# Optimization experiments

Measured on AMD Instinct MI355X. Metric: run time of the kernel, lower is better.

The kernel has to match this reference:

```python
import jax, jax.numpy as jnp
import numpy as np

B, N, C, H, I, ID = 4, 1024, 1024, 16, 77, 768
HD = C // H
HID = 4 * C


def _ln(t, w, b):
    m = jnp.mean(t, axis=-1, keepdims=True)
    v = jnp.mean((t - m) ** 2, axis=-1, keepdims=True)
    return (t - m) * jax.lax.rsqrt(v + 1e-5) * w + b


def _gelu(t):
    return jax.nn.gelu(t, approximate=False)


def setup_inputs() -> dict:
    key = jax.random.key(0)
    ks = iter(jax.random.split(key, 16))

    def nrm(shape, s=0.02):
        return jax.random.normal(next(ks), shape, jnp.float32) * s

    return {
        'x': jax.random.normal(next(ks), (B, N, C), jnp.float32),
        'instruct_states': jax.random.normal(next(ks), (B, I, ID), jnp.float32),
        'norm1_w': jnp.ones((C,), jnp.float32), 'norm1_b': jnp.zeros((C,), jnp.float32),
        'qkv_w': nrm((3 * C, C)),
        'q_bias': jnp.zeros((C,), jnp.float32), 'v_bias': jnp.zeros((C,), jnp.float32),
        'proj_w': nrm((C, C)), 'proj_b': jnp.zeros((C,), jnp.float32),
        'gamma_1': jnp.full((C,), 1e-5, jnp.float32), 'gamma_2': jnp.full((C,), 1e-5, jnp.float32),
        'norm2_w': jnp.ones((C,), jnp.float32), 'norm2_b': jnp.zeros((C,), jnp.float32),
        'fc1_w': nrm((HID, C)), 'fc1_b': jnp.zeros((HID,), jnp.float32),
        'fc2_w': nrm((C, HID)), 'fc2_b': jnp.zeros((C,), jnp.float32),
        'pfc1_w': nrm((HID, C)), 'pfc1_b': jnp.zeros((HID,), jnp.float32),
        'pfc2_w': nrm((C, HID)), 'pfc2_b': jnp.zeros((C,), jnp.float32),
        'parallel_gate': jnp.full((1,), 0.1, jnp.float32),
        'ir_ln_w': jnp.ones((ID,), jnp.float32), 'ir_ln_b': jnp.zeros((ID,), jnp.float32),
        'ir_l1_w': nrm((C, ID)), 'ir_l1_b': jnp.zeros((C,), jnp.float32),
        'ir_l2_w': nrm((C, C)), 'ir_l2_b': jnp.zeros((C,), jnp.float32),
    }


def reference(x, instruct_states, norm1_w, norm1_b, qkv_w, q_bias, v_bias,
              proj_w, proj_b, gamma_1, gamma_2, norm2_w, norm2_b,
              fc1_w, fc1_b, fc2_w, fc2_b, pfc1_w, pfc1_b, pfc2_w, pfc2_b,
              parallel_gate, ir_ln_w, ir_ln_b, ir_l1_w, ir_l1_b, ir_l2_w, ir_l2_b):
    # instruct_dim_reduce: LN -> Linear -> GELU -> Linear
    kv = _ln(instruct_states, ir_ln_w, ir_ln_b)
    kv = _gelu(kv @ ir_l1_w.T + ir_l1_b) @ ir_l2_w.T + ir_l2_b  # [B, I, C]

    xn = _ln(x, norm1_w, norm1_b)                               # [B, N, C]
    cat = jnp.concatenate([kv, xn], axis=1)                     # [B, I+N, C]
    S = I + N

    qkv_bias = jnp.concatenate([q_bias, jnp.zeros_like(v_bias), v_bias])
    qkv = (cat @ qkv_w.T + qkv_bias).reshape(B, S, 3, H, HD)
    q = qkv[:, :, 0].transpose(0, 2, 1, 3)                      # [B, H, S, HD]
    k = qkv[:, :, 1].transpose(0, 2, 1, 3)
    v = qkv[:, :, 2].transpose(0, 2, 1, 3)

    # only visual queries, keys/values over instructions + visual tokens
    q = q[:, :, I:, :] * (HD ** -0.5)                           # [B, H, N, HD]
    attn = jnp.einsum('bhqd,bhkd->bhqk', q, k)                  # [B, H, N, S]
    attn = jax.nn.softmax(attn, axis=-1)
    o = jnp.einsum('bhqk,bhkd->bqhd', attn, v).reshape(B, N, C)
    o = o @ proj_w.T + proj_b

    x = x + gamma_1 * o                                         # LayerScale residual

    y = _ln(x, norm2_w, norm2_b)
    mlp = _gelu(y @ fc1_w.T + fc1_b) @ fc2_w.T + fc2_b
    pmlp = _gelu(y @ pfc1_w.T + pfc1_b) @ pfc2_w.T + pfc2_b
    x = x + gamma_2 * mlp + parallel_gate * pmlp
    return x
```

## Files before the change

kernel.cpp:

```cpp
#include <hip/hip_runtime.h>
#include <cstdint>

#define Bv   4
#define Nv   1024
#define Cv   1024
#define Hv   16
#define Iv   77
#define IDv  768
#define HDv  64
#define HIDv 4096
#define Sv   (Iv + Nv)
#define BIv  (Bv * Iv)
#define BSv  (Bv * Sv)
#define BNv  (Bv * Nv)
#define SPADv 1152

typedef __bf16 bf16x8_t __attribute__((ext_vector_type(8)));
typedef float  f32x4_t  __attribute__((ext_vector_type(4)));
typedef unsigned short us8_t __attribute__((ext_vector_type(8)));
typedef long  l2_t  __attribute__((ext_vector_type(2)));
typedef int   i32x4_t __attribute__((ext_vector_type(4)));
typedef int   i32x8_t __attribute__((ext_vector_type(8)));

__device__ inline f32x4_t zero4() { f32x4_t z; z[0]=0.f; z[1]=0.f; z[2]=0.f; z[3]=0.f; return z; }

__device__ inline unsigned short f2bf(float f) {
    unsigned int u = __builtin_bit_cast(unsigned int, f);
    u = (u + 0x7fffu + ((u >> 16) & 1u)) >> 16;
    return (unsigned short)u;
}
__device__ inline float bf2f(unsigned short u) {
    return __builtin_bit_cast(float, ((unsigned int)u) << 16);
}
__device__ inline unsigned int f4_fp8(float a, float b, float c, float d) {
    int v = __builtin_amdgcn_cvt_pk_fp8_f32(a, b, 0, false);
    v = __builtin_amdgcn_cvt_pk_fp8_f32(c, d, v, true);
    return (unsigned int)v;
}

__device__ inline float gelu_f(float x) {
    float u = 0.7978845608f * x * (1.0f + 0.044715f * x * x);
    float e = __expf(2.0f * u);
    float t = 1.0f - 2.0f / (e + 1.0f);
    return 0.5f * x * (1.0f + t);
}

__device__ inline void gload_lds16(const void* g, void* l) {
    __builtin_amdgcn_global_load_lds(
        (__attribute__((address_space(1))) void*)(unsigned long long)g,
        (__attribute__((address_space(3))) void*)(unsigned long long)l,
        16, 0, 0);
}

__device__ inline i32x8_t frag32(const unsigned char* p0, const unsigned char* p1) {
    i32x4_t lo = *(const i32x4_t*)p0;
    i32x4_t hi = *(const i32x4_t*)p1;
    i32x8_t r;
    r[0] = lo[0]; r[1] = lo[1]; r[2] = lo[2]; r[3] = lo[3];
    r[4] = hi[0]; r[5] = hi[1]; r[6] = hi[2]; r[7] = hi[3];
    return r;
}

#define PIPE_WAIT(N) do { \
    asm volatile("s_waitcnt vmcnt(" #N ")" ::: "memory"); \
    __builtin_amdgcn_s_barrier(); \
    __builtin_amdgcn_sched_barrier(0); \
} while (0)
#define PIPE_RELEASE() do { \
    __builtin_amdgcn_sched_barrier(0); \
    __builtin_amdgcn_s_barrier(); \
} while (0)

__global__ __launch_bounds__(256) void cvt8_kernel(
        const float* s0, const float* s1, const float* s2, const float* s3,
        const float* s4, const float* s5, const float* s6, const float* s7,
        void* d0, void* d1, void* d2, void* d3,
        void* d4, void* d5, void* d6, void* d7,
        const float* g1, const float* g2, const float* gate) {
    long i = (long)blockIdx.x * 256 + threadIdx.x;
    const float* src; void* dst; long off;
    const float* sptr = nullptr; int K4 = 1; float wmul = 1.0f; bool f8 = false;
    if (i < 2097152) {
        if (i < 786432)       { src = s0; dst = d0; off = i; }
        else if (i < 1048576) { src = s1; dst = d1; off = i - 786432;  sptr = g1; K4 = 256; }
        else                  { src = s2; dst = d2; off = i - 1048576; f8 = true; wmul = 32.f; }
    } else if (i < 4194304) {
        if (i < 3145728)      { src = s3; dst = d3; off = i - 2097152; f8 = true; wmul = 32.f; sptr = g2; K4 = 1024; }
        else                  { src = s4; dst = d4; off = i - 3145728; f8 = true; wmul = 32.f; }
    } else {
        if (i < 5242880)      { src = s5; dst = d5; off = i - 4194304; f8 = true; wmul = 32.f; sptr = gate; K4 = 0x7fffffff; }
        else if (i < 5439488) { src = s6; dst = d6; off = i - 5242880; }
        else                  { src = s7; dst = d7; off = i - 5439488; }
    }
    float sc = (sptr ? sptr[(int)(off / K4)] : 1.0f) * wmul;
    float4 v = ((const float4*)src)[off];
    if (f8) {
        ((unsigned int*)dst)[off] = f4_fp8(v.x * sc, v.y * sc, v.z * sc, v.w * sc);
    } else {
        ushort4 o = {f2bf(v.x * sc), f2bf(v.y * sc), f2bf(v.z * sc), f2bf(v.w * sc)};
        ((ushort4*)dst)[off] = o;
    }
}

__global__ __launch_bounds__(256) void bias_prep_kernel(
        const float* __restrict__ qb, const float* __restrict__ vb,
        const float* __restrict__ fc2b, const float* __restrict__ pfc2b,
        const float* __restrict__ projb_in,
        const float* __restrict__ fc1b, const float* __restrict__ pfc1b,
        const float* __restrict__ g1, const float* __restrict__ g2,
        const float* __restrict__ gate,
        float* __restrict__ qkvb, float* __restrict__ bfuse,
        float* __restrict__ projb, float* __restrict__ bcat) {
    int i = blockIdx.x * 256 + threadIdx.x;
    if (i < 3 * Cv) {
        float v = 0.f;
        if (i < Cv) v = qb[i];
        else if (i >= 2 * Cv) v = vb[i - 2 * Cv];
        qkvb[i] = v;
    } else if (i < 4 * Cv) {
        int n = i - 3 * Cv;
        bfuse[n] = g2[n] * fc2b[n] + gate[0] * pfc2b[n];
    } else if (i < 5 * Cv) {
        int n = i - 4 * Cv;
        projb[n] = g1[n] * projb_in[n];
    } else if (i < 13 * Cv) {
        int j = i - 5 * Cv;
        bcat[j] = (j < HIDv) ? fc1b[j] : pfc1b[j - HIDv];
    }
}

__global__ __launch_bounds__(256) void scatter_kv_kernel(const unsigned short* __restrict__ kv,
                                                         unsigned short* __restrict__ cat) {
    int r = blockIdx.x;
    int b = r / Iv, i = r % Iv;
    const uint2* src = (const uint2*)(kv + (size_t)r * Cv);
    uint2* dst = (uint2*)(cat + (size_t)(b * Sv + i) * Cv);
    dst[threadIdx.x] = src[threadIdx.x];
}

template <int F8>
__global__ __launch_bounds__(256) void ln_kernel(const float* __restrict__ in,
                                                 const float* __restrict__ w,
                                                 const float* __restrict__ bvec,
                                                 void* __restrict__ out,
                                                 int cols, float invcols,
                                                 int div_, int stride_, int off_) {
    const int r = blockIdx.x;
    const int tid = threadIdx.x;
    const float* row = in + (size_t)r * cols;
    float s = 0.f, s2 = 0.f;
    for (int c = tid * 4; c < cols; c += 1024) {
        float4 v = *(const float4*)(row + c);
        s  += v.x + v.y + v.z + v.w;
        s2 += v.x * v.x + v.y * v.y + v.z * v.z + v.w * v.w;
    }
#pragma unroll
    for (int o2 = 32; o2 > 0; o2 >>= 1) { s += __shfl_down(s, o2); s2 += __shfl_down(s2, o2); }
    __shared__ float sh[10];
    const int lane = tid & 63, wave = tid >> 6;
    if (lane == 0) { sh[wave] = s; sh[4 + wave] = s2; }
    __syncthreads();
    if (tid == 0) {
        float S1 = sh[0] + sh[1] + sh[2] + sh[3];
        float S2 = sh[4] + sh[5] + sh[6] + sh[7];
        float mean = S1 * invcols;
        float var  = S2 * invcols - mean * mean;
        sh[8] = mean;
        sh[9] = rsqrtf(var + 1e-5f);
    }
    __syncthreads();
    const float mean = sh[8], rstd = sh[9];
    const size_t orow = (size_t)((r / div_) * stride_ + (r % div_) + off_) * cols;
    for (int c = tid * 4; c < cols; c += 1024) {
        float4 v  = *(const float4*)(row + c);
        float4 wv = *(const float4*)(w + c);
        float4 bv = *(const float4*)(bvec + c);
        float o0 = (v.x - mean) * rstd * wv.x + bv.x;
        float o1 = (v.y - mean) * rstd * wv.y + bv.y;
        float o2 = (v.z - mean) * rstd * wv.z + bv.z;
        float o3 = (v.w - mean) * rstd * wv.w + bv.w;
        if constexpr (F8) {
            *(unsigned int*)((unsigned char*)out + orow + c) =
                f4_fp8(o0 * 16.f, o1 * 16.f, o2 * 16.f, o3 * 16.f);
        } else {
            ushort4 o = {f2bf(o0), f2bf(o1), f2bf(o2), f2bf(o3)};
            *(ushort4*)((unsigned short*)out + orow + c) = o;
        }
    }
}

template <int MODE>
__global__ __launch_bounds__(256) void gemm_bf16_kernel(
        const unsigned short* __restrict__ A,
        const unsigned short* __restrict__ W,
        const float* __restrict__ bias,
        unsigned short* __restrict__ outp,
        int M, int N, int K) {
    __shared__ unsigned short As[2][128 * 32];
    __shared__ unsigned short Bs[2][128 * 32];
    const int tid  = threadIdx.x;
    const int lane = tid & 63;
    const int wave = tid >> 6;
    const int m16  = lane & 15;
    const int g4   = lane >> 4;
    const int n0 = blockIdx.x * 128;
    const int m0 = blockIdx.y * 128;
    const int wm = (wave >> 1) * 64;
    const int wn = (wave & 1) * 64;

    const int r0  = tid >> 2;
    const int cc0 = (tid & 3) * 8;
    int am0 = m0 + r0;       if (am0 > M - 1) am0 = M - 1;
    int am1 = m0 + r0 + 64;  if (am1 > M - 1) am1 = M - 1;
    const unsigned short* agp0 = A + (size_t)am0 * K + cc0;
    const unsigned short* agp1 = A + (size_t)am1 * K + cc0;
    const unsigned short* bgp0 = W + (size_t)(n0 + r0) * K + cc0;
    const unsigned short* bgp1 = W + (size_t)(n0 + r0 + 64) * K + cc0;

    f32x4_t acc[4][4];
#pragma unroll
    for (int a = 0; a < 4; ++a)
#pragma unroll
        for (int bb = 0; bb < 4; ++bb) acc[a][bb] = zero4();

    auto stage = [&](int buf) {
        gload_lds16(agp0, &As[buf][wave * 512]);
        gload_lds16(agp1, &As[buf][2048 + wave * 512]);
        gload_lds16(bgp0, &Bs[buf][wave * 512]);
        gload_lds16(bgp1, &Bs[buf][2048 + wave * 512]);
        agp0 += 32; agp1 += 32; bgp0 += 32; bgp1 += 32;
    };

    auto body = [&](int cur) {
        bf16x8_t xf[4], wf[4];
#pragma unroll
        for (int bb = 0; bb < 4; ++bb)
            xf[bb] = *(const bf16x8_t*)&As[cur][(wm + bb * 16 + m16) * 32 + g4 * 8];
#pragma unroll
        for (int a = 0; a < 4; ++a)
            wf[a] = *(const bf16x8_t*)&Bs[cur][(wn + a * 16 + m16) * 32 + g4 * 8];
#pragma unroll
        for (int a = 0; a < 4; ++a)
#pragma unroll
            for (int bb = 0; bb < 4; ++bb)
                acc[a][bb] = __builtin_amdgcn_mfma_f32_16x16x32_bf16(wf[a], xf[bb], acc[a][bb], 0, 0, 0);
    };

    const int NIT = K >> 5;
    stage(0);
    stage(1);
    for (int it = 0; it < NIT - 1; ++it) {
        const int cur = it & 1;
        PIPE_WAIT(4);
        body(cur);
        PIPE_RELEASE();
        if (it + 2 < NIT) stage(cur);
    }
    PIPE_WAIT(0);
    body((NIT - 1) & 1);

#pragma unroll
    for (int a = 0; a < 4; ++a) {
        const int cb = n0 + wn + a * 16 + g4 * 4;
        const float4 bv4 = *(const float4*)(bias + cb);
#pragma unroll
        for (int bb = 0; bb < 4; ++bb) {
            const int r = m0 + wm + bb * 16 + m16;
            if (r < M) {
                const size_t idx = (size_t)r * N + cb;
                const float v0 = acc[a][bb][0] + bv4.x;
                const float v1 = acc[a][bb][1] + bv4.y;
                const float v2 = acc[a][bb][2] + bv4.z;
                const float v3 = acc[a][bb][3] + bv4.w;
                if constexpr (MODE == 0) {
                    ushort4 o = {f2bf(v0), f2bf(v1), f2bf(v2), f2bf(v3)};
                    *(ushort4*)(outp + idx) = o;
                } else {
                    ushort4 o = {f2bf(gelu_f(v0)), f2bf(gelu_f(v1)),
                                 f2bf(gelu_f(v2)), f2bf(gelu_f(v3))};
                    *(ushort4*)(outp + idx) = o;
                }
            }
        }
    }
}

__global__ __launch_bounds__(256) void gemm_splitk_kernel(
        const unsigned short* __restrict__ A1,
        const unsigned short* __restrict__ W1,
        unsigned short* __restrict__ parts,
        int M, int N, int KA, int Kc) {
    __shared__ unsigned short As[2][128 * 32];
    __shared__ unsigned short Bs[2][128 * 32];
    const int tid  = threadIdx.x;
    const int lane = tid & 63;
    const int wave = tid >> 6;
    const int m16  = lane & 15;
    const int g4   = lane >> 4;
    const int bid = blockIdx.x;
    const int xcd = bid & 7, l = bid >> 3;
    const int by = (xcd << 2) | (l & 3);
    const int rr = l >> 2;
    const int bx = rr & 7;
    const int z  = rr >> 3;
    const int n0 = bx * 128;
    const int m0 = by * 128;
    const int wm = (wave >> 1) * 64;
    const int wn = (wave & 1) * 64;
    const int k0 = z * Kc;

    const int r0  = tid >> 2;
    const int cc0 = (tid & 3) * 8;
    const unsigned short* agp0 = A1 + (size_t)(m0 + r0) * KA + k0 + cc0;
    const unsigned short* agp1 = A1 + (size_t)(m0 + r0 + 64) * KA + k0 + cc0;
    const unsigned short* bgp0 = W1 + (size_t)(n0 + r0) * KA + k0 + cc0;
    const unsigned short* bgp1 = W1 + (size_t)(n0 + r0 + 64) * KA + k0 + cc0;

    f32x4_t acc[4][4];
#pragma unroll
    for (int a = 0; a < 4; ++a)
#pragma unroll
        for (int bb = 0; bb < 4; ++bb) acc[a][bb] = zero4();

    auto stage = [&](int buf) {
        gload_lds16(agp0, &As[buf][wave * 512]);
        gload_lds16(agp1, &As[buf][2048 + wave * 512]);
        gload_lds16(bgp0, &Bs[buf][wave * 512]);
        gload_lds16(bgp1, &Bs[buf][2048 + wave * 512]);
        agp0 += 32; agp1 += 32; bgp0 += 32; bgp1 += 32;
    };

    auto body = [&](int cur) {
        bf16x8_t xf[4], wf[4];
#pragma unroll
        for (int bb = 0; bb < 4; ++bb)
            xf[bb] = *(const bf16x8_t*)&As[cur][(wm + bb * 16 + m16) * 32 + g4 * 8];
#pragma unroll
        for (int a = 0; a < 4; ++a)
            wf[a] = *(const bf16x8_t*)&Bs[cur][(wn + a * 16 + m16) * 32 + g4 * 8];
#pragma unroll
        for (int a = 0; a < 4; ++a)
#pragma unroll
            for (int bb = 0; bb < 4; ++bb)
                acc[a][bb] = __builtin_amdgcn_mfma_f32_16x16x32_bf16(wf[a], xf[bb], acc[a][bb], 0, 0, 0);
    };

    const int NIT = Kc >> 5;
    stage(0);
    stage(1);
    for (int it = 0; it < NIT - 1; ++it) {
        const int cur = it & 1;
        PIPE_WAIT(4);
        body(cur);
        PIPE_RELEASE();
        if (it + 2 < NIT) stage(cur);
    }
    PIPE_WAIT(0);
    body((NIT - 1) & 1);

    unsigned short* pz = parts + (size_t)z * M * N;
#pragma unroll
    for (int a = 0; a < 4; ++a) {
        const int cb = n0 + wn + a * 16 + g4 * 4;
#pragma unroll
        for (int bb = 0; bb < 4; ++bb) {
            const int r = m0 + wm + bb * 16 + m16;
            const size_t idx = (size_t)r * N + cb;
            ushort4 o = {f2bf(acc[a][bb][0]), f2bf(acc[a][bb][1]),
                         f2bf(acc[a][bb][2]), f2bf(acc[a][bb][3])};
            *(ushort4*)(pz + idx) = o;
        }
    }
}

__global__ __launch_bounds__(256) void gemm_fp8_gelu_kernel(
        const unsigned char* __restrict__ A,
        const unsigned char* __restrict__ W,
        const float* __restrict__ bias,
        unsigned char* __restrict__ outp,
        int M, int N, int K) {
    __shared__ unsigned char As[2][128 * 128];
    __shared__ unsigned char Bs[2][128 * 128];
    const int tid  = threadIdx.x;
    const int lane = tid & 63;
    const int wave = tid >> 6;
    const int m16  = lane & 15;
    const int g4   = lane >> 4;
    const int bid = blockIdx.x;
    const int xcd = bid & 7, l = bid >> 3;
    const int by = (xcd << 2) | (l & 3);
    const int bx = l >> 2;
    const int n0 = bx * 128;
    const int m0 = by * 128;
    const int wm = (wave >> 1) * 64;
    const int wn = (wave & 1) * 64;

    const int rowin = tid >> 3;
    const int sslot = (tid & 7) ^ (rowin & 7);
    const unsigned char* agp = A + (size_t)(m0 + rowin) * K + sslot * 16;
    const unsigned char* bgp = W + (size_t)(n0 + rowin) * K + sslot * 16;

    const int sw = m16 & 7;
    const int ra0 = ((2 * g4) ^ sw) * 16;
    const int ra1 = ((2 * g4 + 1) ^ sw) * 16;

    f32x4_t acc[4][4];
#pragma unroll
    for (int a = 0; a < 4; ++a)
#pragma unroll
        for (int bb = 0; bb < 4; ++bb) acc[a][bb] = zero4();

    auto stage = [&](int buf) {
#pragma unroll
        for (int j = 0; j < 4; ++j) {
            gload_lds16(agp + (size_t)j * 32 * K, &As[buf][j * 4096 + wave * 1024]);
            gload_lds16(bgp + (size_t)j * 32 * K, &Bs[buf][j * 4096 + wave * 1024]);
        }
        agp += 128; bgp += 128;
    };

    stage(0);
    const int NIT = K >> 7;
    for (int it = 0; it < NIT; ++it) {
        const int cur = it & 1;
        __syncthreads();
        if (it + 1 < NIT) stage(cur ^ 1);
        i32x8_t xv[4], wv[4];
#pragma unroll
        for (int bb = 0; bb < 4; ++bb) {
            const unsigned char* rb = &As[cur][(wm + bb * 16 + m16) * 128];
            xv[bb] = frag32(rb + ra0, rb + ra1);
        }
#pragma unroll
        for (int a = 0; a < 4; ++a) {
            const unsigned char* rb = &Bs[cur][(wn + a * 16 + m16) * 128];
            wv[a] = frag32(rb + ra0, rb + ra1);
        }
#pragma unroll
        for (int a = 0; a < 4; ++a)
#pragma unroll
            for (int bb = 0; bb < 4; ++bb)
                acc[a][bb] = __builtin_amdgcn_mfma_scale_f32_16x16x128_f8f6f4(
                    wv[a], xv[bb], acc[a][bb], 0, 0, 0, 0x7f7f7f7f, 0, 0x7f7f7f7f);
    }

    const float ds = 1.0f / 512.0f;
#pragma unroll
    for (int a = 0; a < 4; ++a) {
        const int cb = n0 + wn + a * 16 + g4 * 4;
        const float4 bv4 = *(const float4*)(bias + cb);
#pragma unroll
        for (int bb = 0; bb < 4; ++bb) {
            const int r = m0 + wm + bb * 16 + m16;
            const size_t idx = (size_t)r * N + cb;
            unsigned int pk = f4_fp8(gelu_f(acc[a][bb][0] * ds + bv4.x) * 16.f,
                                     gelu_f(acc[a][bb][1] * ds + bv4.y) * 16.f,
                                     gelu_f(acc[a][bb][2] * ds + bv4.z) * 16.f,
                                     gelu_f(acc[a][bb][3] * ds + bv4.w) * 16.f);
            *(unsigned int*)(outp + idx) = pk;
        }
    }
}

__global__ __launch_bounds__(256) void gemm_fp8_splitk_kernel(
        const unsigned char* __restrict__ A1,
        const unsigned char* __restrict__ W1,
        const unsigned char* __restrict__ A2,
        const unsigned char* __restrict__ W2,
        unsigned short* __restrict__ parts,
        int M, int N, int lda, int ldw, int Kc, int zsplit) {
    __shared__ unsigned char As[2][128 * 128];
    __shared__ unsigned char Bs[2][128 * 128];
    const int tid  = threadIdx.x;
    const int lane = tid & 63;
    const int wave = tid >> 6;
    const int m16  = lane & 15;
    const int g4   = lane >> 4;
    const int bid = blockIdx.x;
    const int xcd = bid & 7, l = bid >> 3;
    const int by = (xcd << 2) | (l & 3);
    const int rr = l >> 2;
    const int bx = rr & 7;
    const int z  = rr >> 3;
    const int n0 = bx * 128;
    const int m0 = by * 128;
    const int wm = (wave >> 1) * 64;
    const int wn = (wave & 1) * 64;

    const unsigned char* A = (z < zsplit) ? A1 : A2;
    const unsigned char* W = (z < zsplit) ? W1 : W2;
    const int k0 = (z % zsplit) * Kc;

    const int rowin = tid >> 3;
    const int sslot = (tid & 7) ^ (rowin & 7);
    const unsigned char* agp = A + (size_t)(m0 + rowin) * lda + k0 + sslot * 16;
    const unsigned char* bgp = W + (size_t)(n0 + rowin) * ldw + k0 + sslot * 16;

    const int sw = m16 & 7;
    const int ra0 = ((2 * g4) ^ sw) * 16;
    const int ra1 = ((2 * g4 + 1) ^ sw) * 16;

    f32x4_t acc[4][4];
#pragma unroll
    for (int a = 0; a < 4; ++a)
#pragma unroll
        for (int bb = 0; bb < 4; ++bb) acc[a][bb] = zero4();

    auto stage = [&](int buf) {
#pragma unroll
        for (int j = 0; j < 4; ++j) {
            gload_lds16(agp + (size_t)j * 32 * lda, &As[buf][j * 4096 + wave * 1024]);
            gload_lds16(bgp + (size_t)j * 32 * ldw, &Bs[buf][j * 4096 + wave * 1024]);
        }
        agp += 128; bgp += 128;
    };

    stage(0);
    const int NIT = Kc >> 7;
    for (int it = 0; it < NIT; ++it) {
        const int cur = it & 1;
        __syncthreads();
        if (it + 1 < NIT) stage(cur ^ 1);
        i32x8_t xv[4], wv[4];
#pragma unroll
        for (int bb = 0; bb < 4; ++bb) {
            const unsigned char* rb = &As[cur][(wm + bb * 16 + m16) * 128];
            xv[bb] = frag32(rb + ra0, rb + ra1);
        }
#pragma unroll
        for (int a = 0; a < 4; ++a) {
            const unsigned char* rb = &Bs[cur][(wn + a * 16 + m16) * 128];
            wv[a] = frag32(rb + ra0, rb + ra1);
        }
#pragma unroll
        for (int a = 0; a < 4; ++a)
#pragma unroll
            for (int bb = 0; bb < 4; ++bb)
                acc[a][bb] = __builtin_amdgcn_mfma_scale_f32_16x16x128_f8f6f4(
                    wv[a], xv[bb], acc[a][bb], 0, 0, 0, 0x7f7f7f7f, 0, 0x7f7f7f7f);
    }

    unsigned short* pz = parts + (size_t)z * M * N;
    const float ds = 1.0f / 512.0f;
#pragma unroll
    for (int a = 0; a < 4; ++a) {
        const int cb = n0 + wn + a * 16 + g4 * 4;
#pragma unroll
        for (int bb = 0; bb < 4; ++bb) {
            const int r = m0 + wm + bb * 16 + m16;
            const size_t idx = (size_t)r * N + cb;
            ushort4 o = {f2bf(acc[a][bb][0] * ds), f2bf(acc[a][bb][1] * ds),
                         f2bf(acc[a][bb][2] * ds), f2bf(acc[a][bb][3] * ds)};
            *(ushort4*)(pz + idx) = o;
        }
    }
}

template <int NP>
__global__ __launch_bounds__(256) void reduce_kernel(
        const unsigned short* __restrict__ parts,
        const float* __restrict__ resid,
        const float* __restrict__ bias,
        float* __restrict__ out, int MN, int N4mask) {
    int i = blockIdx.x * 256 + threadIdx.x;
    if (i * 4 >= MN) return;
    float4 res = ((const float4*)resid)[i];
    float4 bv  = *(const float4*)(bias + (i & N4mask) * 4);
    float4 o = {res.x + bv.x, res.y + bv.y, res.z + bv.z, res.w + bv.w};
#pragma unroll
    for (int z = 0; z < NP; ++z) {
        ushort4 u = ((const ushort4*)(parts + (size_t)z * MN))[i];
        o.x += bf2f(u.x); o.y += bf2f(u.y); o.z += bf2f(u.z); o.w += bf2f(u.w);
    }
    ((float4*)out)[i] = o;
}

__global__ __launch_bounds__(256) void vtrans_kernel(const unsigned short* __restrict__ qkv,
                                                     unsigned short* __restrict__ vt) {
    __shared__ unsigned short Vs[64 * 64];
    const int stile = blockIdx.x;
    const int bh = blockIdx.y;
    const int b = bh >> 4, h = bh & 15;
    const int tid = threadIdx.x;
#pragma unroll
    for (int j = 0; j < 2; ++j) {
        int c = j * 256 + tid;
        int r = c >> 3, d8 = (c & 7) * 8;
        int s = stile * 64 + r;
        uint4 v = {0u, 0u, 0u, 0u};
        if (s < Sv) v = *(const uint4*)(qkv + ((size_t)(b * Sv + s) * 3 + 2) * Cv + h * 64 + d8);
        *(uint4*)&Vs[r * 64 + d8] = v;
    }
    __syncthreads();
    const int d  = tid >> 2;
    const int p0 = (tid & 3) * 16;
    unsigned short tmp[16];
#pragma unroll
    for (int e = 0; e < 16; ++e) {
        int p = p0 + e;
        int s_local = (p & 32) + 16 * ((p >> 2) & 1) + 4 * ((p & 31) >> 3) + (p & 3);
        tmp[e] = Vs[s_local * 64 + d];
    }
    unsigned short* dst = vt + ((size_t)bh * 64 + d) * SPADv + stile * 64 + p0;
    *(uint4*)dst       = *(const uint4*)&tmp[0];
    *(uint4*)(dst + 8) = *(const uint4*)&tmp[8];
}

__global__ __launch_bounds__(256) void attn_kernel(const unsigned short* __restrict__ qkv,
                                                   const unsigned short* __restrict__ vt,
                                                   unsigned short* __restrict__ o) {
    __shared__ unsigned short Qs[64 * 64];
    __shared__ unsigned short Ks[2][64 * 64];
    __shared__ unsigned short Vts[2][64 * 64];

    const int tid  = threadIdx.x;
    const int lane = tid & 63;
    const int wave = tid >> 6;
    const int m16  = lane & 15;
    const int g4   = lane >> 4;
    const int qt = blockIdx.x;
    const int bh = blockIdx.y;
    const int b = bh >> 4, h = bh & 15;

    const int lr = lane >> 3;
    const int csw = ((lane & 7) ^ lr) * 8;
    const int sw7 = m16 & 7;

#pragma unroll
    for (int j = 0; j < 2; ++j) {
        int r = wave * 16 + j * 8 + lr;
        int s = Iv + qt * 64 + r;
        gload_lds16(qkv + ((size_t)(b * Sv + s) * 3) * Cv + h * 64 + csw,
                    &Qs[(wave * 16 + j * 8) * 64]);
    }

    auto stage_kv = [&](int st, int buf) {
#pragma unroll
        for (int j = 0; j < 2; ++j) {
            int r = wave * 16 + j * 8 + lr;
            int s = st * 64 + r; if (s > Sv - 1) s = Sv - 1;
            gload_lds16(qkv + ((size_t)(b * Sv + s) * 3 + 1) * Cv + h * 64 + csw,
                        &Ks[buf][(wave * 16 + j * 8) * 64]);
            gload_lds16(vt + ((size_t)bh * 64 + r) * SPADv + st * 64 + csw,
                        &Vts[buf][(wave * 16 + j * 8) * 64]);
        }
    };

    f32x4_t oacc[4];
#pragma unroll
    for (int dt = 0; dt < 4; ++dt) oacc[dt] = zero4();
    float m_run = -1e30f, l_run = 0.f;

    stage_kv(0, 0);
    __syncthreads();

    const bf16x8_t qf0 = *(const bf16x8_t*)&Qs[(wave * 16 + m16) * 64 + ((g4 ^ sw7) * 8)];
    const bf16x8_t qf1 = *(const bf16x8_t*)&Qs[(wave * 16 + m16) * 64 + (((4 + g4) ^ sw7) * 8)];

    const int NT = (Sv + 63) / 64;
    for (int st = 0; st < NT; ++st) {
        const int cur = st & 1;
        if (st + 1 < NT) stage_kv(st + 1, cur ^ 1);

        f32x4_t sc[4];
#pragma unroll
        for (int kt = 0; kt < 4; ++kt) {
            bf16x8_t k0 = *(const bf16x8_t*)&Ks[cur][(kt * 16 + m16) * 64 + ((g4 ^ sw7) * 8)];
            bf16x8_t k1 = *(const bf16x8_t*)&Ks[cur][(kt * 16 + m16) * 64 + (((4 + g4) ^ sw7) * 8)];
            f32x4_t z = zero4();
            z = __builtin_amdgcn_mfma_f32_16x16x32_bf16(k0, qf0, z, 0, 0, 0);
            z = __builtin_amdgcn_mfma_f32_16x16x32_bf16(k1, qf1, z, 0, 0, 0);
            sc[kt] = z;
        }

        float mx = -1e30f;
#pragma unroll
        for (int kt = 0; kt < 4; ++kt)
#pragma unroll
            for (int r = 0; r < 4; ++r) {
                int key = st * 64 + kt * 16 + g4 * 4 + r;
                float v = sc[kt][r] * 0.125f;
                v = (key < Sv) ? v : -1e30f;
                sc[kt][r] = v;
                mx = fmaxf(mx, v);
            }
        mx = fmaxf(mx, __shfl_xor(mx, 16));
        mx = fmaxf(mx, __shfl_xor(mx, 32));
        const float mnew  = fmaxf(m_run, mx);
        const float alpha = __expf(m_run - mnew);
        m_run = mnew;
        float sum = 0.f;
#pragma unroll
        for (int kt = 0; kt < 4; ++kt)
#pragma unroll
            for (int r = 0; r < 4; ++r) {
                float p = __expf(sc[kt][r] - mnew);
                sc[kt][r] = p;
                sum += p;
            }
        sum += __shfl_xor(sum, 16);
        sum += __shfl_xor(sum, 32);
        l_run = l_run * alpha + sum;
#pragma unroll
        for (int dt = 0; dt < 4; ++dt) oacc[dt] *= alpha;

        us8_t pu0, pu1;
#pragma unroll
        for (int j = 0; j < 8; ++j) {
            pu0[j] = f2bf(sc[(j >> 2)][j & 3]);
            pu1[j] = f2bf(sc[2 + (j >> 2)][j & 3]);
        }
        const bf16x8_t pf0 = __builtin_bit_cast(bf16x8_t, pu0);
        const bf16x8_t pf1 = __builtin_bit_cast(bf16x8_t, pu1);

#pragma unroll
        for (int dt = 0; dt < 4; ++dt) {
            bf16x8_t v0 = *(const bf16x8_t*)&Vts[cur][(dt * 16 + m16) * 64 + ((g4 ^ sw7) * 8)];
            bf16x8_t v1 = *(const bf16x8_t*)&Vts[cur][(dt * 16 + m16) * 64 + (((4 + g4) ^ sw7) * 8)];
            oacc[dt] = __builtin_amdgcn_mfma_f32_16x16x32_bf16(v0, pf0, oacc[dt], 0, 0, 0);
            oacc[dt] = __builtin_amdgcn_mfma_f32_16x16x32_bf16(v1, pf1, oacc[dt], 0, 0, 0);
        }
        __syncthreads();
    }

    const float inv = 1.0f / l_run;
    const int q = qt * 64 + wave * 16 + m16;
    const size_t row = (size_t)(b * Nv + q) * Cv + h * 64;
#pragma unroll
    for (int dt = 0; dt < 4; ++dt) {
        ushort4 o4 = {f2bf(oacc[dt][0] * inv), f2bf(oacc[dt][1] * inv),
                      f2bf(oacc[dt][2] * inv), f2bf(oacc[dt][3] * inv)};
        *(ushort4*)&o[row + dt * 16 + g4 * 4] = o4;
    }
}

extern "C" void kernel_launch(void* const* d_in, const int* in_sizes, int n_in,
                              void* d_out, int out_size, void* d_ws, size_t ws_size,
                              hipStream_t stream) {
    (void)in_sizes; (void)n_in; (void)out_size; (void)ws_size;
    const float* x       = (const float*)d_in[0];
    const float* instr   = (const float*)d_in[1];
    const float* norm1_w = (const float*)d_in[2];
    const float* norm1_b = (const float*)d_in[3];
    const float* qkv_w   = (const float*)d_in[4];
    const float* q_bias  = (const float*)d_in[5];
    const float* v_bias  = (const float*)d_in[6];
    const float* proj_w  = (const float*)d_in[7];
    const float* proj_b  = (const float*)d_in[8];
    const float* gamma_1 = (const float*)d_in[9];
    const float* gamma_2 = (const float*)d_in[10];
    const float* norm2_w = (const float*)d_in[11];
    const float* norm2_b = (const float*)d_in[12];
    const float* fc1_w   = (const float*)d_in[13];
    const float* fc1_b   = (const float*)d_in[14];
    const float* fc2_w   = (const float*)d_in[15];
    const float* fc2_b   = (const float*)d_in[16];
    const float* pfc1_w  = (const float*)d_in[17];
    const float* pfc1_b  = (const float*)d_in[18];
    const float* pfc2_w  = (const float*)d_in[19];
    const float* pfc2_b  = (const float*)d_in[20];
    const float* gate    = (const float*)d_in[21];
    const float* ir_ln_w = (const float*)d_in[22];
    const float* ir_ln_b = (const float*)d_in[23];
    const float* ir_l1_w = (const float*)d_in[24];
    const float* ir_l1_b = (const float*)d_in[25];
    const float* ir_l2_w = (const float*)d_in[26];
    const float* ir_l2_b = (const float*)d_in[27];
    float* out = (float*)d_out;

    char* ws = (char*)d_ws;
    size_t off = 0;
    auto alloc = [&](size_t bytes) -> char* {
        char* p = ws + off;
        off += (bytes + 255) & ~(size_t)255;
        return p;
    };
    unsigned short* w_qkv  = (unsigned short*)alloc((size_t)3 * Cv * Cv * 2);
    unsigned short* w_proj = (unsigned short*)alloc((size_t)Cv * Cv * 2);
    unsigned char*  w_mlp1 = (unsigned char*)alloc((size_t)2 * HIDv * Cv);
    unsigned char*  w_fc2  = (unsigned char*)alloc((size_t)Cv * HIDv);
    unsigned char*  w_pfc2 = (unsigned char*)alloc((size_t)Cv * HIDv);
    unsigned short* w_ir1  = (unsigned short*)alloc((size_t)Cv * IDv * 2);
    unsigned short* w_ir2  = (unsigned short*)alloc((size_t)Cv * Cv * 2);
    float*          qkvb   = (float*)alloc((size_t)3 * Cv * 4);
    float*          bfuse  = (float*)alloc((size_t)Cv * 4);
    float*          projb  = (float*)alloc((size_t)Cv * 4);
    float*          bcat   = (float*)alloc((size_t)2 * HIDv * 4);
    unsigned short* irln   = (unsigned short*)alloc((size_t)BIv * IDv * 2);
    unsigned short* h1     = (unsigned short*)alloc((size_t)BIv * Cv * 2);
    unsigned short* kvtmp  = (unsigned short*)alloc((size_t)BIv * Cv * 2);
    unsigned short* cat    = (unsigned short*)alloc((size_t)BSv * Cv * 2);
    unsigned short* qkvbuf = (unsigned short*)alloc((size_t)BSv * 3 * Cv * 2);
    unsigned short* obuf   = (unsigned short*)alloc((size_t)BNv * Cv * 2);
    float*          x1     = (float*)alloc((size_t)BNv * Cv * 4);
    unsigned char*  ybuf8  = (unsigned char*)alloc((size_t)BNv * Cv);
    unsigned char*  gbufA  = (unsigned char*)alloc((size_t)BNv * 2 * HIDv);
    unsigned short* fpart  = (unsigned short*)alloc((size_t)4 * BNv * Cv * 2);
    unsigned short* vt     = (unsigned short*)gbufA;
    unsigned short* ppart  = cat;

    cvt8_kernel<<<22272, 256, 0, stream>>>(qkv_w, proj_w, fc1_w, fc2_w, pfc1_w, pfc2_w,
                                           ir_l1_w, ir_l2_w,
                                           w_qkv, w_proj, w_mlp1, w_fc2,
                                           w_mlp1 + (size_t)HIDv * Cv, w_pfc2,
                                           w_ir1, w_ir2,
                                           gamma_1, gamma_2, gate);

    bias_prep_kernel<<<52, 256, 0, stream>>>(q_bias, v_bias, fc2_b, pfc2_b, proj_b,
                                             fc1_b, pfc1_b,
                                             gamma_1, gamma_2, gate,
                                             qkvb, bfuse, projb, bcat);

    ln_kernel<0><<<BIv, 256, 0, stream>>>(instr, ir_ln_w, ir_ln_b, irln,
                                          IDv, 1.0f / IDv, 1 << 28, 0, 0);
    ln_kernel<0><<<BNv, 256, 0, stream>>>(x, norm1_w, norm1_b, cat,
                                          Cv, 1.0f / Cv, Nv, Sv, Iv);
    gemm_bf16_kernel<1><<<dim3(Cv / 128, (BIv + 127) / 128), 256, 0, stream>>>(
        irln, w_ir1, ir_l1_b, h1, BIv, Cv, IDv);
    gemm_bf16_kernel<0><<<dim3(Cv / 128, (BIv + 127) / 128), 256, 0, stream>>>(
        h1, w_ir2, ir_l2_b, kvtmp, BIv, Cv, Cv);
    scatter_kv_kernel<<<BIv, 256, 0, stream>>>(kvtmp, cat);

    gemm_bf16_kernel<0><<<dim3(3 * Cv / 128, (BSv + 127) / 128), 256, 0, stream>>>(
        cat, w_qkv, qkvb, qkvbuf, BSv, 3 * Cv, Cv);

    vtrans_kernel<<<dim3(18, Bv * Hv), 256, 0, stream>>>(qkvbuf, vt);
    attn_kernel<<<dim3(Nv / 64, Bv * Hv), 256, 0, stream>>>(qkvbuf, vt, obuf);

    gemm_splitk_kernel<<<1024, 256, 0, stream>>>(
        obuf, w_proj, ppart, BNv, Cv, Cv, Cv / 4);
    reduce_kernel<4><<<(BNv * Cv / 4 + 255) / 256, 256, 0, stream>>>(
        ppart, x, projb, x1, BNv * Cv, Cv / 4 - 1);

    ln_kernel<1><<<BNv, 256, 0, stream>>>(x1, norm2_w, norm2_b, ybuf8,
                                          Cv, 1.0f / Cv, 1 << 28, 0, 0);

    gemm_fp8_gelu_kernel<<<2048, 256, 0, stream>>>(
        ybuf8, w_mlp1, bcat, gbufA, BNv, 2 * HIDv, Cv);

    gemm_fp8_splitk_kernel<<<1024, 256, 0, stream>>>(
        gbufA, w_fc2, gbufA + HIDv, w_pfc2, fpart,
        BNv, Cv, 2 * HIDv, HIDv, HIDv / 2, 2);
    reduce_kernel<4><<<(BNv * Cv / 4 + 255) / 256, 256, 0, stream>>>(
        fpart, x1, bfuse, out, BNv * Cv, Cv / 4 - 1);
}
```

Before: 483.2 us.

## Switch QKV and output-projection GEMMs from bf16 to fp8 MFMA

Converts the QKV and proj weights to scaled fp8. The LN1 output, the scattered instruction kv and the attention output are now written as fp8 with a x16 scale. A new fp8 GEMM with bf16 output handles the QKV projection, and the proj GEMM reuses the existing fp8 split-k kernel. gamma_1 is moved from the weight conversion into a new reduce_scale kernel. This halves operand bytes and uses the higher-throughput fp8 MFMA, at the cost of lower precision on the attention path.

```diff
diff --git a/kernel.cpp b/kernel.cpp
--- a/kernel.cpp
+++ b/kernel.cpp
@@ -77,12 +77,13 @@
         void* d0, void* d1, void* d2, void* d3,
         void* d4, void* d5, void* d6, void* d7,
         const float* g1, const float* g2, const float* gate) {
+    (void)g1;
     long i = (long)blockIdx.x * 256 + threadIdx.x;
     const float* src; void* dst; long off;
     const float* sptr = nullptr; int K4 = 1; float wmul = 1.0f; bool f8 = false;
     if (i < 2097152) {
-        if (i < 786432)       { src = s0; dst = d0; off = i; }
-        else if (i < 1048576) { src = s1; dst = d1; off = i - 786432;  sptr = g1; K4 = 256; }
+        if (i < 786432)       { src = s0; dst = d0; off = i; f8 = true; wmul = 32.f; }
+        else if (i < 1048576) { src = s1; dst = d1; off = i - 786432;  f8 = true; wmul = 32.f; }
         else                  { src = s2; dst = d2; off = i - 1048576; f8 = true; wmul = 32.f; }
     } else if (i < 4194304) {
         if (i < 3145728)      { src = s3; dst = d3; off = i - 2097152; f8 = true; wmul = 32.f; sptr = g2; K4 = 1024; }
@@ -130,12 +131,14 @@
 }
 
 __global__ __launch_bounds__(256) void scatter_kv_kernel(const unsigned short* __restrict__ kv,
-                                                         unsigned short* __restrict__ cat) {
+                                                         unsigned char* __restrict__ cat) {
     int r = blockIdx.x;
     int b = r / Iv, i = r % Iv;
-    const uint2* src = (const uint2*)(kv + (size_t)r * Cv);
-    uint2* dst = (uint2*)(cat + (size_t)(b * Sv + i) * Cv);
-    dst[threadIdx.x] = src[threadIdx.x];
+    const ushort4* src = (const ushort4*)(kv + (size_t)r * Cv);
+    unsigned int* dst = (unsigned int*)(cat + (size_t)(b * Sv + i) * Cv);
+    ushort4 u = src[threadIdx.x];
+    dst[threadIdx.x] = f4_fp8(bf2f(u.x) * 16.f, bf2f(u.y) * 16.f,
+                              bf2f(u.z) * 16.f, bf2f(u.w) * 16.f);
 }
 
 template <int F8>
@@ -285,36 +288,37 @@
     }
 }
 
-__global__ __launch_bounds__(256) void gemm_splitk_kernel(
-        const unsigned short* __restrict__ A1,
-        const unsigned short* __restrict__ W1,
-        unsigned short* __restrict__ parts,
-        int M, int N, int KA, int Kc) {
-    __shared__ unsigned short As[2][128 * 32];
-    __shared__ unsigned short Bs[2][128 * 32];
+__global__ __launch_bounds__(256) void gemm_fp8_bf16out_kernel(
+        const unsigned char* __restrict__ A,
+        const unsigned char* __restrict__ W,
+        const float* __restrict__ bias,
+        unsigned short* __restrict__ outp,
+        int M, int N, int K) {
+    __shared__ unsigned char As[2][128 * 128];
+    __shared__ unsigned char Bs[2][128 * 128];
     const int tid  = threadIdx.x;
     const int lane = tid & 63;
     const int wave = tid >> 6;
     const int m16  = lane & 15;
     const int g4   = lane >> 4;
-    const int bid = blockIdx.x;
-    const int xcd = bid & 7, l = bid >> 3;
-    const int by = (xcd << 2) | (l & 3);
-    const int rr = l >> 2;
-    const int bx = rr & 7;
-    const int z  = rr >> 3;
-    const int n0 = bx * 128;
-    const int m0 = by * 128;
+    const int n0 = blockIdx.x * 128;
+    const int m0 = blockIdx.y * 128;
     const int wm = (wave >> 1) * 64;
     const int wn = (wave & 1) * 64;
-    const int k0 = z * Kc;
-
-    const int r0  = tid >> 2;
-    const int cc0 = (tid & 3) * 8;
-    const unsigned short* agp0 = A1 + (size_t)(m0 + r0) * KA + k0 + cc0;
-    const unsigned short* agp1 = A1 + (size_t)(m0 + r0 + 64) * KA + k0 + cc0;
-    const unsigned short* bgp0 = W1 + (size_t)(n0 + r0) * KA + k0 + cc0;
-    const unsigned short* bgp1 = W1 + (size_t)(n0 + r0 + 64) * KA + k0 + cc0;
+
+    const int rowin = tid >> 3;
+    const int sslot = (tid & 7) ^ (rowin & 7);
+    const unsigned char* agp[4];
+#pragma unroll
+    for (int j = 0; j < 4; ++j) {
+        int gr = m0 + j * 32 + rowin; if (gr > M - 1) gr = M - 1;
+        agp[j] = A + (size_t)gr * K + sslot * 16;
+    }
+    const unsigned char* bgp = W + (size_t)(n0 + rowin) * K + sslot * 16;
+
+    const int sw = m16 & 7;
+    const int ra0 = ((2 * g4) ^ sw) * 16;
+    const int ra1 = ((2 * g4 + 1) ^ sw) * 16;
 
     f32x4_t acc[4][4];
 #pragma unroll
@@ -323,52 +327,56 @@
         for (int bb = 0; bb < 4; ++bb) acc[a][bb] = zero4();
 
     auto stage = [&](int buf) {
-        gload_lds16(agp0, &As[buf][wave * 512]);
-        gload_lds16(agp1, &As[buf][2048 + wave * 512]);
-        gload_lds16(bgp0, &Bs[buf][wave * 512]);
-        gload_lds16(bgp1, &Bs[buf][2048 + wave * 512]);
-        agp0 += 32; agp1 += 32; bgp0 += 32; bgp1 += 32;
+#pragma unroll
+        for (int j = 0; j < 4; ++j) {
+            gload_lds16(agp[j], &As[buf][j * 4096 + wave * 1024]);
+            gload_lds16(bgp + (size_t)j * 32 * K, &Bs[buf][j * 4096 + wave * 1024]);
+            agp[j] += 128;
+        }
+        bgp += 128;
     };
 
-    auto body = [&](int cur) {
-        bf16x8_t xf[4], wf[4];
-#pragma unroll
-        for (int bb = 0; bb < 4; ++bb)
-            xf[bb] = *(const bf16x8_t*)&As[cur][(wm + bb * 16 + m16) * 32 + g4 * 8];
+    stage(0);
+    const int NIT = K >> 7;
+    for (int it = 0; it < NIT; ++it) {
+        const int cur = it & 1;
+        __syncthreads();
+        if (it + 1 < NIT) stage(cur ^ 1);
+        i32x8_t xv[4], wv[4];
+#pragma unroll
+        for (int bb = 0; bb < 4; ++bb) {
+            const unsigned char* rb = &As[cur][(wm + bb * 16 + m16) * 128];
+            xv[bb] = frag32(rb + ra0, rb + ra1);
+        }
+#pragma unroll
+        for (int a = 0; a < 4; ++a) {
+            const unsigned char* rb = &Bs[cur][(wn + a * 16 + m16) * 128];
+            wv[a] = frag32(rb + ra0, rb + ra1);
+        }
 #pragma unroll
         for (int a = 0; a < 4; ++a)
-            wf[a] = *(const bf16x8_t*)&Bs[cur][(wn + a * 16 + m16) * 32 + g4 * 8];
-#pragma unroll
-        for (int a = 0; a < 4; ++a)
 #pragma unroll
             for (int bb = 0; bb < 4; ++bb)
-                acc[a][bb] = __builtin_amdgcn_mfma_f32_16x16x32_bf16(wf[a], xf[bb], acc[a][bb], 0, 0, 0);
-    };
-
-    const int NIT = Kc >> 5;
-    stage(0);
-    stage(1);
-    for (int it = 0; it < NIT - 1; ++it) {
-        const int cur = it & 1;
-        PIPE_WAIT(4);
-        body(cur);
-        PIPE_RELEASE();
-        if (it + 2 < NIT) stage(cur);
-    }
-    PIPE_WAIT(0);
-    body((NIT - 1) & 1);
-
-    unsigned short* pz = parts + (size_t)z * M * N;
+                acc[a][bb] = __builtin_amdgcn_mfma_scale_f32_16x16x128_f8f6f4(
+                    wv[a], xv[bb], acc[a][bb], 0, 0, 0, 0x7f7f7f7f, 0, 0x7f7f7f7f);
+    }
+
+    const float ds = 1.0f / 512.0f;
 #pragma unroll
     for (int a = 0; a < 4; ++a) {
         const int cb = n0 + wn + a * 16 + g4 * 4;
+        const float4 bv4 = *(const float4*)(bias + cb);
 #pragma unroll
         for (int bb = 0; bb < 4; ++bb) {
             const int r = m0 + wm + bb * 16 + m16;
-            const size_t idx = (size_t)r * N + cb;
-            ushort4 o = {f2bf(acc[a][bb][0]), f2bf(acc[a][bb][1]),
-                         f2bf(acc[a][bb][2]), f2bf(acc[a][bb][3])};
-            *(ushort4*)(pz + idx) = o;
+            if (r < M) {
+                const size_t idx = (size_t)r * N + cb;
+                ushort4 o = {f2bf(acc[a][bb][0] * ds + bv4.x),
+                             f2bf(acc[a][bb][1] * ds + bv4.y),
+                             f2bf(acc[a][bb][2] * ds + bv4.z),
+                             f2bf(acc[a][bb][3] * ds + bv4.w)};
+                *(ushort4*)(outp + idx) = o;
+            }
         }
     }
 }
@@ -575,6 +583,30 @@
     ((float4*)out)[i] = o;
 }
 
+template <int NP>
+__global__ __launch_bounds__(256) void reduce_scale_kernel(
+        const unsigned short* __restrict__ parts,
+        const float* __restrict__ resid,
+        const float* __restrict__ bias,
+        const float* __restrict__ scale,
+        float* __restrict__ out, int MN, int N4mask) {
+    int i = blockIdx.x * 256 + threadIdx.x;
+    if (i * 4 >= MN) return;
+    float4 res = ((const float4*)resid)[i];
+    const int c4 = (i & N4mask) * 4;
+    float4 bv = *(const float4*)(bias + c4);
+    float4 sc = *(const float4*)(scale + c4);
+    float sx = 0.f, sy = 0.f, sz = 0.f, sw = 0.f;
+#pragma unroll
+    for (int z = 0; z < NP; ++z) {
+        ushort4 u = ((const ushort4*)(parts + (size_t)z * MN))[i];
+        sx += bf2f(u.x); sy += bf2f(u.y); sz += bf2f(u.z); sw += bf2f(u.w);
+    }
+    float4 o = {res.x + bv.x + sc.x * sx, res.y + bv.y + sc.y * sy,
+                res.z + bv.z + sc.z * sz, res.w + bv.w + sc.w * sw};
+    ((float4*)out)[i] = o;
+}
+
 __global__ __launch_bounds__(256) void vtrans_kernel(const unsigned short* __restrict__ qkv,
                                                      unsigned short* __restrict__ vt) {
     __shared__ unsigned short Vs[64 * 64];
@@ -608,7 +640,7 @@
 
 __global__ __launch_bounds__(256) void attn_kernel(const unsigned short* __restrict__ qkv,
                                                    const unsigned short* __restrict__ vt,
-                                                   unsigned short* __restrict__ o) {
+                                                   unsigned char* __restrict__ o) {
     __shared__ unsigned short Qs[64 * 64];
     __shared__ unsigned short Ks[2][64 * 64];
     __shared__ unsigned short Vts[2][64 * 64];
@@ -723,14 +755,14 @@
         __syncthreads();
     }
 
-    const float inv = 1.0f / l_run;
+    const float inv16 = 16.0f / l_run;
     const int q = qt * 64 + wave * 16 + m16;
     const size_t row = (size_t)(b * Nv + q) * Cv + h * 64;
 #pragma unroll
     for (int dt = 0; dt < 4; ++dt) {
-        ushort4 o4 = {f2bf(oacc[dt][0] * inv), f2bf(oacc[dt][1] * inv),
-                      f2bf(oacc[dt][2] * inv), f2bf(oacc[dt][3] * inv)};
-        *(ushort4*)&o[row + dt * 16 + g4 * 4] = o4;
+        *(unsigned int*)&o[row + dt * 16 + g4 * 4] =
+            f4_fp8(oacc[dt][0] * inv16, oacc[dt][1] * inv16,
+                   oacc[dt][2] * inv16, oacc[dt][3] * inv16);
     }
 }
 
@@ -775,8 +807,8 @@
         off += (bytes + 255) & ~(size_t)255;
         return p;
     };
-    unsigned short* w_qkv  = (unsigned short*)alloc((size_t)3 * Cv * Cv * 2);
-    unsigned short* w_proj = (unsigned short*)alloc((size_t)Cv * Cv * 2);
+    unsigned char*  w_qkv8 = (unsigned char*)alloc((size_t)3 * Cv * Cv);
+    unsigned char*  w_proj8= (unsigned char*)alloc((size_t)Cv * Cv);
     unsigned char*  w_mlp1 = (unsigned char*)alloc((size_t)2 * HIDv * Cv);
     unsigned char*  w_fc2  = (unsigned char*)alloc((size_t)Cv * HIDv);
     unsigned char*  w_pfc2 = (unsigned char*)alloc((size_t)Cv * HIDv);
@@ -789,19 +821,19 @@
     unsigned short* irln   = (unsigned short*)alloc((size_t)BIv * IDv * 2);
     unsigned short* h1     = (unsigned short*)alloc((size_t)BIv * Cv * 2);
     unsigned short* kvtmp  = (unsigned short*)alloc((size_t)BIv * Cv * 2);
-    unsigned short* cat    = (unsigned short*)alloc((size_t)BSv * Cv * 2);
+    unsigned char*  cat8   = (unsigned char*)alloc((size_t)BSv * Cv);
     unsigned short* qkvbuf = (unsigned short*)alloc((size_t)BSv * 3 * Cv * 2);
-    unsigned short* obuf   = (unsigned short*)alloc((size_t)BNv * Cv * 2);
+    unsigned char*  obuf8  = (unsigned char*)alloc((size_t)BNv * Cv);
     float*          x1     = (float*)alloc((size_t)BNv * Cv * 4);
     unsigned char*  ybuf8  = (unsigned char*)alloc((size_t)BNv * Cv);
     unsigned char*  gbufA  = (unsigned char*)alloc((size_t)BNv * 2 * HIDv);
     unsigned short* fpart  = (unsigned short*)alloc((size_t)4 * BNv * Cv * 2);
     unsigned short* vt     = (unsigned short*)gbufA;
-    unsigned short* ppart  = cat;
+    unsigned short* ppart  = fpart;
 
     cvt8_kernel<<<22272, 256, 0, stream>>>(qkv_w, proj_w, fc1_w, fc2_w, pfc1_w, pfc2_w,
                                            ir_l1_w, ir_l2_w,
-                                           w_qkv, w_proj, w_mlp1, w_fc2,
+                                           w_qkv8, w_proj8, w_mlp1, w_fc2,
                                            w_mlp1 + (size_t)HIDv * Cv, w_pfc2,
                                            w_ir1, w_ir2,
                                            gamma_1, gamma_2, gate);
@@ -813,24 +845,25 @@
 
     ln_kernel<0><<<BIv, 256, 0, stream>>>(instr, ir_ln_w, ir_ln_b, irln,
                                           IDv, 1.0f / IDv, 1 << 28, 0, 0);
-    ln_kernel<0><<<BNv, 256, 0, stream>>>(x, norm1_w, norm1_b, cat,
+    ln_kernel<1><<<BNv, 256, 0, stream>>>(x, norm1_w, norm1_b, cat8,
                                           Cv, 1.0f / Cv, Nv, Sv, Iv);
     gemm_bf16_kernel<1><<<dim3(Cv / 128, (BIv + 127) / 128), 256, 0, stream>>>(
         irln, w_ir1, ir_l1_b, h1, BIv, Cv, IDv);
     gemm_bf16_kernel<0><<<dim3(Cv / 128, (BIv + 127) / 128), 256, 0, stream>>>(
         h1, w_ir2, ir_l2_b, kvtmp, BIv, Cv, Cv);
-    scatter_kv_kernel<<<BIv, 256, 0, stream>>>(kvtmp, cat);
-
-    gemm_bf16_kernel<0><<<dim3(3 * Cv / 128, (BSv + 127) / 128), 256, 0, stream>>>(
-        cat, w_qkv, qkvb, qkvbuf, BSv, 3 * Cv, Cv);
+    scatter_kv_kernel<<<BIv, 256, 0, stream>>>(kvtmp, cat8);
+
+    gemm_fp8_bf16out_kernel<<<dim3(3 * Cv / 128, (BSv + 127) / 128), 256, 0, stream>>>(
+        cat8, w_qkv8, qkvb, qkvbuf, BSv, 3 * Cv, Cv);
 
     vtrans_kernel<<<dim3(18, Bv * Hv), 256, 0, stream>>>(qkvbuf, vt);
-    attn_kernel<<<dim3(Nv / 64, Bv * Hv), 256, 0, stream>>>(qkvbuf, vt, obuf);
-
-    gemm_splitk_kernel<<<1024, 256, 0, stream>>>(
-        obuf, w_proj, ppart, BNv, Cv, Cv, Cv / 4);
-    reduce_kernel<4><<<(BNv * Cv / 4 + 255) / 256, 256, 0, stream>>>(
-        ppart, x, projb, x1, BNv * Cv, Cv / 4 - 1);
+    attn_kernel<<<dim3(Nv / 64, Bv * Hv), 256, 0, stream>>>(qkvbuf, vt, obuf8);
+
+    gemm_fp8_splitk_kernel<<<1024, 256, 0, stream>>>(
+        obuf8, w_proj8, obuf8, w_proj8, ppart,
+        BNv, Cv, Cv, Cv, Cv / 4, 4);
+    reduce_scale_kernel<4><<<(BNv * Cv / 4 + 255) / 256, 256, 0, stream>>>(
+        ppart, x, projb, gamma_1, x1, BNv * Cv, Cv / 4 - 1);
 
     ln_kernel<1><<<BNv, 256, 0, stream>>>(x1, norm2_w, norm2_b, ybuf8,
                                           Cv, 1.0f / Cv, 1 << 28, 0, 0);
```

New measurement: 436.8 us. 1.11x faster.
